# Optimization experiments

Measured on AMD Instinct MI355X. Metric: run time of the kernel, lower is better.

## Reference

```python
import jax, jax.numpy as jnp
import numpy as np

B, S, D = 4, 2048, 1024
H = 16
DK = D // H  # 64
F = 4096


def layer_norm(x, g, b, eps=1e-5):
    mu = jnp.mean(x, axis=-1, keepdims=True)
    var = jnp.mean(jnp.square(x - mu), axis=-1, keepdims=True)
    return (x - mu) * jax.lax.rsqrt(var + eps) * g + b


def setup_inputs() -> dict:
    key = jax.random.key(0)
    ks = jax.random.split(key, 12)
    s_in = 1.0 / np.sqrt(D)
    s_ff = 1.0 / np.sqrt(F)
    return {
        "x": jax.random.normal(ks[0], (B, S, D), jnp.float32),
        # per-head Q/K/V projections stacked: [H, D, DK]
        "Wq": jax.random.normal(ks[1], (H, D, DK), jnp.float32) * s_in,
        "bq": jnp.zeros((H, DK), jnp.float32),
        "Wk": jax.random.normal(ks[2], (H, D, DK), jnp.float32) * s_in,
        "bk": jnp.zeros((H, DK), jnp.float32),
        "Wv": jax.random.normal(ks[3], (H, D, DK), jnp.float32) * s_in,
        "bv": jnp.zeros((H, DK), jnp.float32),
        # output projection: [H*DK, D]
        "Wo": jax.random.normal(ks[4], (H * DK, D), jnp.float32) * s_in,
        "bo": jnp.zeros((D,), jnp.float32),
        "ln1_g": jnp.ones((D,), jnp.float32),
        "ln1_b": jnp.zeros((D,), jnp.float32),
        # FFN
        "W1": jax.random.normal(ks[5], (D, F), jnp.float32) * s_in,
        "b1": jnp.zeros((F,), jnp.float32),
        "W2": jax.random.normal(ks[6], (F, D), jnp.float32) * s_ff,
        "b2": jnp.zeros((D,), jnp.float32),
        "ln2_g": jnp.ones((D,), jnp.float32),
        "ln2_b": jnp.zeros((D,), jnp.float32),
    }


def reference(x, Wq, bq, Wk, bk, Wv, bv, Wo, bo, ln1_g, ln1_b,
              W1, b1, W2, b2, ln2_g, ln2_b):
    # --- multi-head attention (self-attention: q = k = v = x) ---
    q = jnp.einsum("bsd,hdk->bhsk", x, Wq) + bq[:, None, :]
    k = jnp.einsum("bsd,hdk->bhsk", x, Wk) + bk[:, None, :]
    v = jnp.einsum("bsd,hdk->bhsk", x, Wv) + bv[:, None, :]
    scale = 1.0 / jnp.sqrt(jnp.asarray(DK, x.dtype))
    scores = jnp.einsum("bhsk,bhtk->bhst", q, k) * scale  # [B,H,S,S]
    attn = jax.nn.softmax(scores, axis=-1)
    ctx = jnp.einsum("bhst,bhtk->bhsk", attn, v)           # [B,H,S,DK]
    # concat heads -> [B,S,H*DK], output projection
    ctx = jnp.transpose(ctx, (0, 2, 1, 3)).reshape(B, S, H * DK)
    attn_out = ctx @ Wo + bo
    # residual + post-LN (dropout is identity in eval mode)
    h = layer_norm(x + attn_out, ln1_g, ln1_b)
    # --- feed-forward (tanh activation) ---
    ff = jnp.tanh(h @ W1 + b1) @ W2 + b2
    return layer_norm(h + ff, ln2_g, ln2_b)
```

## Files before the change

kernel.cpp:

```cpp
#include <hip/hip_runtime.h>
#include <hip/hip_bf16.h>
#include <math.h>

typedef __attribute__((ext_vector_type(8))) short short8;
typedef __attribute__((ext_vector_type(4))) float f32x4;

#define NB 4
#define NS 2048
#define ND 1024
#define NH 16
#define NDK 64
#define NF 4096
#define NM (NB*NS)

#define QSCALE 0.18033688f

__device__ __forceinline__ unsigned short f2b(float f) {
  union { __hip_bfloat16 h; unsigned short u; } c;
  c.h = __float2bfloat16(f);
  return c.u;
}

__device__ __forceinline__ float b2f(unsigned short u) {
  union { float f; unsigned int i; } c;
  c.i = ((unsigned int)u) << 16;
  return c.f;
}

__device__ __forceinline__ void gload_lds16(const void* g, void* l) {
  __builtin_amdgcn_global_load_lds((const __attribute__((address_space(1))) void*)g,
                                   (__attribute__((address_space(3))) void*)l,
                                   16, 0, 0);
}

__device__ __forceinline__ float fast_tanh(float x) {
  float e = __builtin_amdgcn_exp2f(x * 2.885390082f);
  return 1.0f - 2.0f * __builtin_amdgcn_rcpf(e + 1.0f);
}

#define PREP_NBLK 20492

__global__ __launch_bounds__(256)
void prep_all(const float* __restrict__ x, unsigned short* __restrict__ x_bf,
              const float* __restrict__ Wq, const float* __restrict__ Wk,
              const float* __restrict__ Wv, unsigned short* __restrict__ Wqkvt,
              const float* __restrict__ Wo, unsigned short* __restrict__ Wot,
              const float* __restrict__ W1, unsigned short* __restrict__ W1t,
              const float* __restrict__ W2, unsigned short* __restrict__ W2t,
              const float* __restrict__ bq, const float* __restrict__ bk,
              const float* __restrict__ bv, float* __restrict__ bqkv)
{
  __shared__ float t[32][33];
  const int bid = blockIdx.x;
  const int tid = threadIdx.x;
  const int tx = tid & 31, ty = tid >> 5;

  if (bid < 8192) {
    int i = bid * 256 + tid;
    float4 v = ((const float4*)x)[i];
    ushort4 o;
    o.x = f2b(v.x); o.y = f2b(v.y); o.z = f2b(v.z); o.w = f2b(v.w);
    ((ushort4*)x_bf)[i] = o;
    return;
  }
  if (bid < 11264) {
    int idx = bid - 8192;
    int z = idx >> 6, y = (idx >> 5) & 1, xb = idx & 31;
    int which = z / 16, h = z % 16;
    const float* src = (which == 0 ? Wq : which == 1 ? Wk : Wv) + (size_t)h * ND * NDK;
    float scale = (which == 0) ? QSCALE : 1.0f;
    unsigned short* d = Wqkvt + (size_t)(which * 1024 + h * 64) * ND;
    int k0 = xb * 32, n0 = y * 32;
    for (int r = ty; r < 32; r += 8)
      t[r][tx] = src[(size_t)(k0 + r) * NDK + n0 + tx];
    __syncthreads();
    for (int r = ty; r < 32; r += 8)
      d[(size_t)(n0 + r) * ND + k0 + tx] = f2b(t[tx][r] * scale);
    return;
  }
  const float* src; unsigned short* dst; int ldsrc, lddst, k0, n0;
  if (bid < 12288) {
    int idx = bid - 11264; src = Wo; dst = Wot; ldsrc = 1024; lddst = 1024;
    k0 = (idx & 31) * 32; n0 = (idx >> 5) * 32;
  } else if (bid < 16384) {
    int idx = bid - 12288; src = W1; dst = W1t; ldsrc = 4096; lddst = 1024;
    k0 = (idx & 31) * 32; n0 = (idx >> 5) * 32;
  } else if (bid < 20480) {
    int idx = bid - 16384; src = W2; dst = W2t; ldsrc = 1024; lddst = 4096;
    k0 = (idx >> 5) * 32; n0 = (idx & 31) * 32;
  } else {
    int i = (bid - 20480) * 256 + tid;
    if (i < 3072) {
      float v = (i < 1024) ? bq[i] * QSCALE : (i < 2048 ? bk[i - 1024] : bv[i - 2048]);
      bqkv[i] = v;
    }
    return;
  }
  for (int r = ty; r < 32; r += 8)
    t[r][tx] = src[(size_t)(k0 + r) * ldsrc + n0 + tx];
  __syncthreads();
  for (int r = ty; r < 32; r += 8)
    dst[(size_t)(n0 + r) * lddst + k0 + tx] = f2b(t[tx][r]);
}

__global__ __launch_bounds__(256)
void transpose_v(const unsigned short* __restrict__ qkv, unsigned short* __restrict__ vt) {
  __shared__ unsigned short t[32][33];
  int bh = blockIdx.z; int b = bh >> 4, h = bh & 15;
  int s0 = blockIdx.x * 32;
  int d0 = blockIdx.y * 32;
  int tx = threadIdx.x, ty = threadIdx.y;
  for (int r = ty; r < 32; r += 8)
    t[r][tx] = qkv[(size_t)(b * NS + s0 + r) * 3072 + 2048 + h * 64 + d0 + tx];
  __syncthreads();
  for (int r = ty; r < 32; r += 8)
    vt[((size_t)bh * 64 + d0 + r) * NS + s0 + tx] = t[tx][r];
}


template<int EPI>
__global__ __launch_bounds__(512, 1)
void gemm_bt(const unsigned short* __restrict__ A, const unsigned short* __restrict__ Bt,
             const float* __restrict__ bias, void* __restrict__ Cout,
             int M, int N, int K)
{
  __shared__ __align__(16) unsigned short As[2][256 * 64];
  __shared__ __align__(16) unsigned short Bs[2][128 * 64];

  const int nwg = gridDim.x;
  const int id = blockIdx.x;
  const int swz = (id & 7) * (nwg >> 3) + (id >> 3);
  const int nbx = N >> 7;
  const int mb = swz / nbx, nb = swz % nbx;
  const int m0 = mb * 256;
  const int n0 = nb * 128;

  const int tid = threadIdx.x;
  const int wave = tid >> 6, lane = tid & 63;
  const int l16 = lane & 15, lhi = lane >> 4;
  const int wr = wave >> 1, wc = wave & 1;

  const int rowL = lane >> 3;
  const int gg = (lane & 7) ^ rowL;

  f32x4 acc[4][4] = {};

  auto STAGE = [&](int buf, int kt) {
    const int k0 = kt * 64;
#pragma unroll
    for (int c = wave * 4; c < wave * 4 + 4; ++c)
      gload_lds16(A + (size_t)(m0 + c * 8 + rowL) * K + (k0 + gg * 8), &As[buf][c * 512]);
#pragma unroll
    for (int c = wave * 2; c < wave * 2 + 2; ++c)
      gload_lds16(Bt + (size_t)(n0 + c * 8 + rowL) * K + (k0 + gg * 8), &Bs[buf][c * 512]);
  };

  auto COMPUTE = [&](int buf) {
    const char* as = (const char*)&As[buf][0];
    const char* bs = (const char*)&Bs[buf][0];
    short8 af[4][2], bf[4][2];
#pragma unroll
    for (int i = 0; i < 4; ++i) {
      const int row = wr * 64 + i * 16 + l16;
      const char* rb = as + row * 128;
#pragma unroll
      for (int ks = 0; ks < 2; ++ks)
        af[i][ks] = *(const short8*)(rb + (((ks * 4 + lhi) ^ (row & 7)) << 4));
    }
#pragma unroll
    for (int j = 0; j < 4; ++j) {
      const int row = wc * 64 + j * 16 + l16;
      const char* rb = bs + row * 128;
#pragma unroll
      for (int ks = 0; ks < 2; ++ks)
        bf[j][ks] = *(const short8*)(rb + (((ks * 4 + lhi) ^ (row & 7)) << 4));
    }
    __builtin_amdgcn_s_setprio(1);
#pragma unroll
    for (int i = 0; i < 4; ++i)
#pragma unroll
      for (int j = 0; j < 4; ++j)
#pragma unroll
        for (int ks = 0; ks < 2; ++ks)
          acc[i][j] = __builtin_amdgcn_mfma_f32_16x16x32_bf16(af[i][ks], bf[j][ks],
                                                              acc[i][j], 0, 0, 0);
    __builtin_amdgcn_s_setprio(0);
  };

  const int NT = K >> 6;
  STAGE(0, 0);
  __syncthreads();
  for (int j = 0; j < NT; j += 2) {
    STAGE(1, j + 1);
    COMPUTE(0);
    __syncthreads();
    if (j + 2 < NT) STAGE(0, j + 2);
    COMPUTE(1);
    __syncthreads();
  }

#pragma unroll
  for (int i = 0; i < 4; ++i) {
    const int row = m0 + wr * 64 + i * 16 + lhi * 4;
#pragma unroll
    for (int j = 0; j < 4; ++j) {
      const int col = n0 + wc * 64 + j * 16 + l16;
      const float bv = bias[col];
#pragma unroll
      for (int r = 0; r < 4; ++r) {
        float v = acc[i][j][r] + bv;
        size_t idx = (size_t)(row + r) * N + col;
        if (EPI == 0)      ((unsigned short*)Cout)[idx] = f2b(v);
        else if (EPI == 1) ((float*)Cout)[idx] = v;
        else               ((unsigned short*)Cout)[idx] = f2b(fast_tanh(v));
      }
    }
  }
}


template<int EPI>
__global__ __launch_bounds__(512, 2)
void gemm256(const unsigned short* __restrict__ A, const unsigned short* __restrict__ Bt,
             const float* __restrict__ bias, void* __restrict__ Cout,
             int M, int N, int K)
{
  __shared__ __align__(16) unsigned short As[2][256 * 64];
  __shared__ __align__(16) unsigned short Bs[2][256 * 64];

  const int nwg = gridDim.x;
  const int id = blockIdx.x;
  const int swz = (id & 7) * (nwg >> 3) + (id >> 3);
  const int nbx = N >> 8;
  const int mb = swz / nbx, nb = swz % nbx;
  const int m0 = mb * 256;
  const int n0 = nb * 256;

  const int tid = threadIdx.x;
  const int wave = tid >> 6, lane = tid & 63;
  const int l16 = lane & 15, lhi = lane >> 4;
  const int wr = wave >> 2, wc = wave & 3;

  const int rowL = lane >> 3;
  const int gg = (lane & 7) ^ rowL;

  f32x4 acc[8][4] = {};

  auto STAGE = [&](int buf, int kt) {
    const int k0 = kt * 64;
#pragma unroll
    for (int c = wave * 4; c < wave * 4 + 4; ++c) {
      gload_lds16(A + (size_t)(m0 + c * 8 + rowL) * K + (k0 + gg * 8), &As[buf][c * 512]);
      gload_lds16(Bt + (size_t)(n0 + c * 8 + rowL) * K + (k0 + gg * 8), &Bs[buf][c * 512]);
    }
  };

  auto COMPUTE = [&](int buf) {
    const char* as = (const char*)&As[buf][0];
    const char* bs = (const char*)&Bs[buf][0];
    short8 bf[4][2];
#pragma unroll
    for (int j = 0; j < 4; ++j) {
      const int row = wc * 64 + j * 16 + l16;
      const char* rb = bs + row * 128;
#pragma unroll
      for (int ks = 0; ks < 2; ++ks)
        bf[j][ks] = *(const short8*)(rb + (((ks * 4 + lhi) ^ (row & 7)) << 4));
    }
#pragma unroll
    for (int i = 0; i < 8; ++i) {
      const int row = wr * 128 + i * 16 + l16;
      const char* rb = as + row * 128;
      short8 af[2];
#pragma unroll
      for (int ks = 0; ks < 2; ++ks)
        af[ks] = *(const short8*)(rb + (((ks * 4 + lhi) ^ (row & 7)) << 4));
      __builtin_amdgcn_s_setprio(1);
#pragma unroll
      for (int j = 0; j < 4; ++j)
#pragma unroll
        for (int ks = 0; ks < 2; ++ks)
          acc[i][j] = __builtin_amdgcn_mfma_f32_16x16x32_bf16(af[ks], bf[j][ks],
                                                              acc[i][j], 0, 0, 0);
      __builtin_amdgcn_s_setprio(0);
    }
  };

  const int NT = K >> 6;
  STAGE(0, 0);
  __syncthreads();
  for (int j = 0; j < NT; j += 2) {
    STAGE(1, j + 1);
    COMPUTE(0);
    __syncthreads();
    if (j + 2 < NT) STAGE(0, j + 2);
    COMPUTE(1);
    __syncthreads();
  }

#pragma unroll
  for (int i = 0; i < 8; ++i) {
    const int row = m0 + wr * 128 + i * 16 + lhi * 4;
#pragma unroll
    for (int j = 0; j < 4; ++j) {
      const int col = n0 + wc * 64 + j * 16 + l16;
      const float bv = bias[col];
#pragma unroll
      for (int r = 0; r < 4; ++r) {
        float v = acc[i][j][r] + bv;
        size_t idx = (size_t)(row + r) * N + col;
        if (EPI == 0)      ((unsigned short*)Cout)[idx] = f2b(v);
        else if (EPI == 1) ((float*)Cout)[idx] = v;
        else               ((unsigned short*)Cout)[idx] = f2b(fast_tanh(v));
      }
    }
  }
}


__global__ __launch_bounds__(512)
void attn_fwd(const unsigned short* __restrict__ qkv, const unsigned short* __restrict__ vtg,
              unsigned short* __restrict__ ctx)
{
  const int id = blockIdx.x;
  const int swz = (id & 7) * 128 + (id >> 3);
  const int qt = swz & 15;
  const int bh = swz >> 4;
  const int b = bh >> 4, h = bh & 15;
  const int row0 = b * NS + qt * 128;
  const int tid = threadIdx.x;
  const int wave = tid >> 6, lane = tid & 63;
  const int l16 = lane & 15, lhi = lane >> 4;

  __shared__ __align__(16) unsigned short Ks[2][64 * 64];
  __shared__ __align__(16) unsigned short Vs[2][64 * 64];
  __shared__ __align__(16) unsigned short Ps[8][16 * 64];

  const unsigned short* kbase = qkv + ND + (size_t)h * 64;
  const unsigned short* vbase = vtg + (size_t)bh * 64 * NS;

  const int r0 = tid >> 3;
  const int f0 = ((tid & 7) ^ (r0 & 7)) * 8;
  const int ldsb0 = wave * 512;

  const int lbase = l16 * 128;
  const int xs = (l16 & 7) << 4;
  const int kvo0 = (lhi * 16) ^ xs;
  const int kvo1 = (64 + lhi * 16) ^ xs;
  int pjo[4];
#pragma unroll
  for (int j = 0; j < 4; ++j)
    pjo[j] = (j * 32 + lhi * 8) ^ xs;

  short8 ones8;
#pragma unroll
  for (int e = 0; e < 8; ++e) ones8[e] = (short)0x3F80;

  short8 qf[2];
  {
    const unsigned short* qrow = qkv + (size_t)(row0 + wave * 16 + l16) * 3072 + h * 64;
    qf[0] = *(const short8*)(qrow + lhi * 8);
    qf[1] = *(const short8*)(qrow + 32 + lhi * 8);
  }

  f32x4 o[4] = {};
  f32x4 o5 = {};

  auto STAGE = [&](int buf, int kt) {
    const size_t kr = (size_t)(b * NS + kt * 64);
    const int kb64 = kt * 64;
    gload_lds16(kbase + (kr + r0) * 3072 + f0, &Ks[buf][ldsb0]);
    gload_lds16(vbase + (size_t)r0 * NS + kb64 + f0, &Vs[buf][ldsb0]);
  };

  auto COMPUTE = [&](int buf) {
    const char* kb = (const char*)&Ks[buf][0];
    const char* vb = (const char*)&Vs[buf][0];
    char* pb = (char*)&Ps[wave][0];

    f32x4 s[4] = {};
    __builtin_amdgcn_s_setprio(1);
#pragma unroll
    for (int c = 0; c < 2; ++c) {
      const int kvo = c ? kvo1 : kvo0;
#pragma unroll
      for (int j = 0; j < 4; ++j) {
        short8 kf = *(const short8*)(kb + lbase + j * 2048 + kvo);
        s[j] = __builtin_amdgcn_mfma_f32_16x16x32_bf16(kf, qf[c], s[j], 0, 0, 0);
      }
    }
    __builtin_amdgcn_s_setprio(0);

#pragma unroll
    for (int j = 0; j < 4; ++j) {
#pragma unroll
      for (int r = 0; r < 4; ++r)
        s[j][r] = __builtin_amdgcn_exp2f(s[j][r]);
      unsigned int lo = (unsigned int)f2b(s[j][0]) | ((unsigned int)f2b(s[j][1]) << 16);
      unsigned int hi = (unsigned int)f2b(s[j][2]) | ((unsigned int)f2b(s[j][3]) << 16);
      unsigned long long w = (unsigned long long)lo | ((unsigned long long)hi << 32);
      *(unsigned long long*)(pb + lbase + pjo[j]) = w;
    }

    __builtin_amdgcn_s_setprio(1);
#pragma unroll
    for (int c = 0; c < 2; ++c) {
      const int kvo = c ? kvo1 : kvo0;
      short8 pf = *(const short8*)(pb + lbase + kvo);
#pragma unroll
      for (int j = 0; j < 4; ++j) {
        short8 vf = *(const short8*)(vb + lbase + j * 2048 + kvo);
        o[j] = __builtin_amdgcn_mfma_f32_16x16x32_bf16(pf, vf, o[j], 0, 0, 0);
      }
      o5 = __builtin_amdgcn_mfma_f32_16x16x32_bf16(pf, ones8, o5, 0, 0, 0);
    }
    __builtin_amdgcn_s_setprio(0);
  };

  STAGE(0, 0);
  __syncthreads();
  for (int kt = 0; kt < NS / 64; kt += 2) {
    STAGE(1, kt + 1);
    COMPUTE(0);
    __syncthreads();
    if (kt + 2 < NS / 64) STAGE(0, kt + 2);
    COMPUTE(1);
    __syncthreads();
  }

  float rinv[4];
#pragma unroll
  for (int r = 0; r < 4; ++r) rinv[r] = 1.0f / o5[r];
#pragma unroll
  for (int j = 0; j < 4; ++j)
#pragma unroll
    for (int r = 0; r < 4; ++r) {
      const int row = row0 + wave * 16 + lhi * 4 + r;
      ctx[(size_t)row * ND + h * 64 + j * 16 + l16] = f2b(o[j][r] * rinv[r]);
    }
}


template<int OUTF32>
__global__ __launch_bounds__(256)
void ln_fused(const unsigned short* __restrict__ xa, const unsigned short* __restrict__ xb,
              const float* __restrict__ g, const float* __restrict__ beta, void* out_)
{
  const int row = blockIdx.x;
  const int tid = threadIdx.x;
  const int wave = tid >> 6, lane = tid & 63;
  __shared__ float r1[4], r2[4];

  ushort4 au = ((const ushort4*)(xa + (size_t)row * ND))[tid];
  ushort4 bu = ((const ushort4*)(xb + (size_t)row * ND))[tid];
  float v0 = b2f(au.x) + b2f(bu.x), v1 = b2f(au.y) + b2f(bu.y);
  float v2 = b2f(au.z) + b2f(bu.z), v3 = b2f(au.w) + b2f(bu.w);

  float sm = v0 + v1 + v2 + v3;
#pragma unroll
  for (int d = 1; d < 64; d <<= 1) sm += __shfl_xor(sm, d);
  if (lane == 0) r1[wave] = sm;
  __syncthreads();
  const float mu = (r1[0] + r1[1] + r1[2] + r1[3]) * (1.0f / ND);
  const float d0 = v0 - mu, d1 = v1 - mu, d2 = v2 - mu, d3 = v3 - mu;
  float vs = d0 * d0 + d1 * d1 + d2 * d2 + d3 * d3;
#pragma unroll
  for (int d = 1; d < 64; d <<= 1) vs += __shfl_xor(vs, d);
  if (lane == 0) r2[wave] = vs;
  __syncthreads();
  const float var = (r2[0] + r2[1] + r2[2] + r2[3]) * (1.0f / ND);
  const float inv = rsqrtf(var + 1e-5f);
  float4 gg = ((const float4*)g)[tid];
  float4 bb = ((const float4*)beta)[tid];
  float o0 = d0 * inv * gg.x + bb.x;
  float o1 = d1 * inv * gg.y + bb.y;
  float o2 = d2 * inv * gg.z + bb.z;
  float o3 = d3 * inv * gg.w + bb.w;
  if (OUTF32 == 0) {
    ushort4 w; w.x = f2b(o0); w.y = f2b(o1); w.z = f2b(o2); w.w = f2b(o3);
    ((ushort4*)((unsigned short*)out_ + (size_t)row * ND))[tid] = w;
  } else {
    float4 ov; ov.x = o0; ov.y = o1; ov.z = o2; ov.w = o3;
    ((float4*)((float*)out_ + (size_t)row * ND))[tid] = ov;
  }
}


extern "C" void kernel_launch(void* const* d_in, const int* in_sizes, int n_in,
                              void* d_out, int out_size, void* d_ws, size_t ws_size,
                              hipStream_t stream)
{
  (void)in_sizes; (void)n_in; (void)out_size; (void)ws_size;
  const float* x   = (const float*)d_in[0];
  const float* Wq  = (const float*)d_in[1];
  const float* bq  = (const float*)d_in[2];
  const float* Wk  = (const float*)d_in[3];
  const float* bk  = (const float*)d_in[4];
  const float* Wv  = (const float*)d_in[5];
  const float* bv  = (const float*)d_in[6];
  const float* Wo  = (const float*)d_in[7];
  const float* bo  = (const float*)d_in[8];
  const float* g1  = (const float*)d_in[9];
  const float* be1 = (const float*)d_in[10];
  const float* W1  = (const float*)d_in[11];
  const float* b1  = (const float*)d_in[12];
  const float* W2  = (const float*)d_in[13];
  const float* b2  = (const float*)d_in[14];
  const float* g2  = (const float*)d_in[15];
  const float* be2 = (const float*)d_in[16];

  char* ws = (char*)d_ws;
  const size_t MB = 1ull << 20;
  unsigned short* x_bf  = (unsigned short*)(ws);
  unsigned short* qkv   = (unsigned short*)(ws + 16 * MB);
  unsigned short* aout  = (unsigned short*)(ws + 16 * MB);
  unsigned short* ff1   = (unsigned short*)(ws);
  unsigned short* ctx   = (unsigned short*)(ws + 64 * MB);
  unsigned short* h_bf  = (unsigned short*)(ws + 64 * MB);
  unsigned short* Wqkvt = (unsigned short*)(ws + 80 * MB);
  unsigned short* Wot   = (unsigned short*)(ws + 86 * MB);
  unsigned short* W1t   = (unsigned short*)(ws + 88 * MB);
  unsigned short* W2t   = (unsigned short*)(ws + 96 * MB);
  float*          bqkv  = (float*)(ws + 104 * MB);
  unsigned short* ffout = (unsigned short*)(ws + 105 * MB);
  unsigned short* vtg   = (unsigned short*)(ws + 121 * MB);

  prep_all<<<PREP_NBLK, 256, 0, stream>>>(x, x_bf, Wq, Wk, Wv, Wqkvt,
                                          Wo, Wot, W1, W1t, W2, W2t,
                                          bq, bk, bv, bqkv);

  gemm_bt<0><<<(NM / 256) * (3072 / 128), 512, 0, stream>>>(x_bf, Wqkvt, bqkv, qkv, NM, 3072, 1024);
  transpose_v<<<dim3(64, 2, 64), dim3(32, 8), 0, stream>>>(qkv, vtg);
  attn_fwd<<<1024, 512, 0, stream>>>(qkv, vtg, ctx);
  gemm_bt<0><<<(NM / 256) * (1024 / 128), 512, 0, stream>>>(ctx, Wot, bo, aout, NM, 1024, 1024);
  ln_fused<0><<<NM, 256, 0, stream>>>(x_bf, aout, g1, be1, h_bf);
  gemm256<2><<<(NM / 256) * (4096 / 256), 512, 0, stream>>>(h_bf, W1t, b1, ff1, NM, 4096, 1024);
  gemm_bt<0><<<(NM / 256) * (1024 / 128), 512, 0, stream>>>(ff1, W2t, b2, ffout, NM, 1024, 4096);
  ln_fused<1><<<NM, 256, 0, stream>>>(h_bf, ffout, g2, be2, (float*)d_out);
}
```

Before: 420.3 us.

## Double attention query tile per block to reuse staged K/V tiles

Each attention block now processes 256 query rows instead of 128, with every wave handling two 16-row sub-tiles that share each K and V fragment loaded from LDS. This halves the number of blocks and halves the global K/V traffic per query, and doubles the MFMA work per LDS read. In exchange it raises register use (two sets of score and output accumulators) and LDS for the P buffers, and the grid shrinks to 512 blocks, which may leave the 256 CUs less evenly loaded.

```diff
diff --git a/kernel.cpp b/kernel.cpp
--- a/kernel.cpp
+++ b/kernel.cpp
@@ -323,18 +323,18 @@
               unsigned short* __restrict__ ctx)
 {
   const int id = blockIdx.x;
-  const int swz = (id & 7) * 128 + (id >> 3);
-  const int qt = swz & 15;
-  const int bh = swz >> 4;
+  const int swz = (id & 7) * 64 + (id >> 3);
+  const int qt = swz & 7;
+  const int bh = swz >> 3;
   const int b = bh >> 4, h = bh & 15;
-  const int row0 = b * NS + qt * 128;
+  const int row0 = b * NS + qt * 256;
   const int tid = threadIdx.x;
   const int wave = tid >> 6, lane = tid & 63;
   const int l16 = lane & 15, lhi = lane >> 4;
 
   __shared__ __align__(16) unsigned short Ks[2][64 * 64];
   __shared__ __align__(16) unsigned short Vs[2][64 * 64];
-  __shared__ __align__(16) unsigned short Ps[8][16 * 64];
+  __shared__ __align__(16) unsigned short Ps[16][16 * 64];
 
   const unsigned short* kbase = qkv + ND + (size_t)h * 64;
   const unsigned short* vbase = vtg + (size_t)bh * 64 * NS;
@@ -356,15 +356,17 @@
 #pragma unroll
   for (int e = 0; e < 8; ++e) ones8[e] = (short)0x3F80;
 
-  short8 qf[2];
-  {
-    const unsigned short* qrow = qkv + (size_t)(row0 + wave * 16 + l16) * 3072 + h * 64;
-    qf[0] = *(const short8*)(qrow + lhi * 8);
-    qf[1] = *(const short8*)(qrow + 32 + lhi * 8);
-  }
-
-  f32x4 o[4] = {};
-  f32x4 o5 = {};
+  short8 qf[2][2];
+#pragma unroll
+  for (int sub = 0; sub < 2; ++sub) {
+    const unsigned short* qrow =
+        qkv + (size_t)(row0 + wave * 32 + sub * 16 + l16) * 3072 + h * 64;
+    qf[sub][0] = *(const short8*)(qrow + lhi * 8);
+    qf[sub][1] = *(const short8*)(qrow + 32 + lhi * 8);
+  }
+
+  f32x4 o[2][4] = {};
+  f32x4 o5[2] = {};
 
   auto STAGE = [&](int buf, int kt) {
     const size_t kr = (size_t)(b * NS + kt * 64);
@@ -376,9 +378,10 @@
   auto COMPUTE = [&](int buf) {
     const char* kb = (const char*)&Ks[buf][0];
     const char* vb = (const char*)&Vs[buf][0];
-    char* pb = (char*)&Ps[wave][0];
-
-    f32x4 s[4] = {};
+    char* pb0 = (char*)&Ps[wave * 2 + 0][0];
+    char* pb1 = (char*)&Ps[wave * 2 + 1][0];
+
+    f32x4 s[2][4] = {};
     __builtin_amdgcn_s_setprio(1);
 #pragma unroll
     for (int c = 0; c < 2; ++c) {
@@ -386,33 +389,41 @@
 #pragma unroll
       for (int j = 0; j < 4; ++j) {
         short8 kf = *(const short8*)(kb + lbase + j * 2048 + kvo);
-        s[j] = __builtin_amdgcn_mfma_f32_16x16x32_bf16(kf, qf[c], s[j], 0, 0, 0);
+        s[0][j] = __builtin_amdgcn_mfma_f32_16x16x32_bf16(kf, qf[0][c], s[0][j], 0, 0, 0);
+        s[1][j] = __builtin_amdgcn_mfma_f32_16x16x32_bf16(kf, qf[1][c], s[1][j], 0, 0, 0);
       }
     }
     __builtin_amdgcn_s_setprio(0);
 
 #pragma unroll
-    for (int j = 0; j < 4; ++j) {
-#pragma unroll
-      for (int r = 0; r < 4; ++r)
-        s[j][r] = __builtin_amdgcn_exp2f(s[j][r]);
-      unsigned int lo = (unsigned int)f2b(s[j][0]) | ((unsigned int)f2b(s[j][1]) << 16);
-      unsigned int hi = (unsigned int)f2b(s[j][2]) | ((unsigned int)f2b(s[j][3]) << 16);
-      unsigned long long w = (unsigned long long)lo | ((unsigned long long)hi << 32);
-      *(unsigned long long*)(pb + lbase + pjo[j]) = w;
+    for (int sub = 0; sub < 2; ++sub) {
+      char* pb = sub ? pb1 : pb0;
+#pragma unroll
+      for (int j = 0; j < 4; ++j) {
+#pragma unroll
+        for (int r = 0; r < 4; ++r)
+          s[sub][j][r] = __builtin_amdgcn_exp2f(s[sub][j][r]);
+        unsigned int lo = (unsigned int)f2b(s[sub][j][0]) | ((unsigned int)f2b(s[sub][j][1]) << 16);
+        unsigned int hi = (unsigned int)f2b(s[sub][j][2]) | ((unsigned int)f2b(s[sub][j][3]) << 16);
+        unsigned long long w = (unsigned long long)lo | ((unsigned long long)hi << 32);
+        *(unsigned long long*)(pb + lbase + pjo[j]) = w;
+      }
     }
 
     __builtin_amdgcn_s_setprio(1);
 #pragma unroll
     for (int c = 0; c < 2; ++c) {
       const int kvo = c ? kvo1 : kvo0;
-      short8 pf = *(const short8*)(pb + lbase + kvo);
+      short8 pf0 = *(const short8*)(pb0 + lbase + kvo);
+      short8 pf1 = *(const short8*)(pb1 + lbase + kvo);
 #pragma unroll
       for (int j = 0; j < 4; ++j) {
         short8 vf = *(const short8*)(vb + lbase + j * 2048 + kvo);
-        o[j] = __builtin_amdgcn_mfma_f32_16x16x32_bf16(pf, vf, o[j], 0, 0, 0);
+        o[0][j] = __builtin_amdgcn_mfma_f32_16x16x32_bf16(pf0, vf, o[0][j], 0, 0, 0);
+        o[1][j] = __builtin_amdgcn_mfma_f32_16x16x32_bf16(pf1, vf, o[1][j], 0, 0, 0);
       }
-      o5 = __builtin_amdgcn_mfma_f32_16x16x32_bf16(pf, ones8, o5, 0, 0, 0);
+      o5[0] = __builtin_amdgcn_mfma_f32_16x16x32_bf16(pf0, ones8, o5[0], 0, 0, 0);
+      o5[1] = __builtin_amdgcn_mfma_f32_16x16x32_bf16(pf1, ones8, o5[1], 0, 0, 0);
     }
     __builtin_amdgcn_s_setprio(0);
   };
@@ -428,16 +439,19 @@
     __syncthreads();
   }
 
-  float rinv[4];
-#pragma unroll
-  for (int r = 0; r < 4; ++r) rinv[r] = 1.0f / o5[r];
-#pragma unroll
-  for (int j = 0; j < 4; ++j)
-#pragma unroll
-    for (int r = 0; r < 4; ++r) {
-      const int row = row0 + wave * 16 + lhi * 4 + r;
-      ctx[(size_t)row * ND + h * 64 + j * 16 + l16] = f2b(o[j][r] * rinv[r]);
-    }
+#pragma unroll
+  for (int sub = 0; sub < 2; ++sub) {
+    float rinv[4];
+#pragma unroll
+    for (int r = 0; r < 4; ++r) rinv[r] = 1.0f / o5[sub][r];
+#pragma unroll
+    for (int j = 0; j < 4; ++j)
+#pragma unroll
+      for (int r = 0; r < 4; ++r) {
+        const int row = row0 + wave * 32 + sub * 16 + lhi * 4 + r;
+        ctx[(size_t)row * ND + h * 64 + j * 16 + l16] = f2b(o[sub][j][r] * rinv[r]);
+      }
+  }
 }
 
 
@@ -531,7 +545,7 @@
 
   gemm_bt<0><<<(NM / 256) * (3072 / 128), 512, 0, stream>>>(x_bf, Wqkvt, bqkv, qkv, NM, 3072, 1024);
   transpose_v<<<dim3(64, 2, 64), dim3(32, 8), 0, stream>>>(qkv, vtg);
-  attn_fwd<<<1024, 512, 0, stream>>>(qkv, vtg, ctx);
+  attn_fwd<<<512, 512, 0, stream>>>(qkv, vtg, ctx);
   gemm_bt<0><<<(NM / 256) * (1024 / 128), 512, 0, stream>>>(ctx, Wot, bo, aout, NM, 1024, 1024);
   ln_fused<0><<<NM, 256, 0, stream>>>(x_bf, aout, g1, be1, h_bf);
   gemm256<2><<<(NM / 256) * (4096 / 256), 512, 0, stream>>>(h_bf, W1t, b1, ff1, NM, 4096, 1024);
```

Measured after the change: 407.8 us. -3.0%, faster.
